# Kernel optimization log

Hardware: AMD Instinct MI355X
Metric: run time of the kernel (lower is better)

Reference implementation:

```python
import jax, jax.numpy as jnp
import numpy as np

N, E, F_IN, H, C, L = 100000, 1600000, 128, 64, 16, 3
NEG_SLOPE_ATT = 0.2   # GATConv attention leaky_relu
NEG_SLOPE_ACT = 0.01  # F.leaky_relu default


def setup_inputs() -> dict:
    key = jax.random.key(0)
    ks = jax.random.split(key, 12)
    x = jax.random.normal(ks[0], (N, F_IN), dtype=jnp.float32)
    edge_index = jax.random.randint(ks[1], (2, E), 0, N, dtype=jnp.int64)
    edge_weight = jax.random.uniform(ks[2], (E,), dtype=jnp.float32)
    s = 0.05
    W_in = jax.random.normal(ks[3], (F_IN, H), dtype=jnp.float32) * s
    b_in = jnp.zeros((H,), dtype=jnp.float32)
    Wc = jax.random.normal(ks[4], (L, H, H), dtype=jnp.float32) * s
    a_src = jax.random.normal(ks[5], (L, H), dtype=jnp.float32) * s
    a_dst = jax.random.normal(ks[6], (L, H), dtype=jnp.float32) * s
    bc = jnp.zeros((L, H), dtype=jnp.float32)
    W_out = jax.random.normal(ks[7], (H, C), dtype=jnp.float32) * s
    b_out = jnp.zeros((C,), dtype=jnp.float32)
    return {"x": x, "edge_index": edge_index, "edge_weight": edge_weight,
            "W_in": W_in, "b_in": b_in, "Wc": Wc, "a_src": a_src,
            "a_dst": a_dst, "bc": bc, "W_out": W_out, "b_out": b_out}


def _gat_layer(h, src, dst, W, asrc, adst, b):
    # linear transform (no bias on lin in PyG GATConv)
    h = h @ W                                   # [N, H]
    # per-node attention contributions
    alpha_s = h @ asrc                          # [N]
    alpha_d = h @ adst                          # [N]
    e = jax.nn.leaky_relu(alpha_s[src] + alpha_d[dst], NEG_SLOPE_ATT)  # [E']
    # segment softmax over destination nodes
    m = jax.ops.segment_max(e, dst, num_segments=N)
    ex = jnp.exp(e - m[dst])
    denom = jax.ops.segment_sum(ex, dst, num_segments=N)
    w = ex / (denom[dst] + 1e-16)
    # weighted scatter-add aggregation
    out = jax.ops.segment_sum(h[src] * w[:, None], dst, num_segments=N)
    return out + b


def reference(x, edge_index, edge_weight, W_in, b_in, Wc, a_src, a_dst, bc, W_out, b_out):
    # add self-loops (PyG GATConv default)
    loops = jnp.arange(N, dtype=edge_index.dtype)
    src = jnp.concatenate([edge_index[0], loops])
    dst = jnp.concatenate([edge_index[1], loops])

    h = jax.nn.leaky_relu(x @ W_in + b_in, NEG_SLOPE_ACT)
    for l in range(L):
        h = jax.nn.leaky_relu(_gat_layer(h, src, dst, Wc[l], a_src[l], a_dst[l], bc[l]), NEG_SLOPE_ACT)
    logits = h @ W_out + b_out
    return jax.nn.log_softmax(logits, axis=-1)
```

## Files before the change

kernel.cpp:

```cpp
#include <hip/hip_runtime.h>

#define N_NODES 100000
#define E_EDGES 1600000
#define F_IN    128
#define H_DIM   64
#define C_OUT   16
#define L_LAYERS 3
#define NTOT    (E_EDGES + N_NODES)
#define MAXD    64

#define BKN2    512
#define NB2     ((N_NODES + BKN2 - 1) / BKN2)
#define BCAP    9216
#define CH      8192
#define PB      ((E_EDGES + CH - 1) / CH)

typedef __attribute__((ext_vector_type(8))) short short8;
typedef __attribute__((ext_vector_type(4))) float f32x4;

__device__ inline unsigned short f2bf(float f) {
    unsigned u = __float_as_uint(f);
    return (unsigned short)((u + 0x7FFFu + ((u >> 16) & 1u)) >> 16);
}
__device__ inline float bf_lo(unsigned p) { return __uint_as_float(p << 16); }
__device__ inline float bf_hi(unsigned p) { return __uint_as_float(p & 0xFFFF0000u); }
__device__ inline unsigned cvt_pk_bf16(float lo, float hi) {
    unsigned r;
    asm("v_cvt_pk_bf16_f32 %0, %1, %2" : "=v"(r) : "v"(lo), "v"(hi));
    return r;
}

__global__ __launch_bounds__(256) void bucket_scatter2(
        const void* __restrict__ eidx,
        int* __restrict__ bcur, unsigned int* __restrict__ packed) {
    __shared__ int cnt[NB2], basel[NB2], curl[NB2], gbase[NB2];
    __shared__ int sd[256];
    __shared__ int sflag;
    __shared__ unsigned int stage[CH];
    __shared__ unsigned char bkt[CH];
    int t = threadIdx.x;
    int b0 = blockIdx.x * CH;
    int ne = min(CH, E_EDGES - b0);
    if (t == 0) sflag = 0;
    for (int i = t; i < NB2; i += 256) cnt[i] = 0;
    __syncthreads();
    {
        int nsamp = min(ne, 1024);
        int any = 0;
        for (int j = t; j < nsamp; j += 256)
            if (((const unsigned*)eidx)[2 * (size_t)(b0 + j) + 1] != 0u) any = 1;
        if (any) atomicOr(&sflag, 1);
    }
    __syncthreads();
    int f64 = sflag ? 0 : 1;

    int es[CH / 256], ed[CH / 256];
    #pragma unroll
    for (int j = 0; j < CH / 256; ++j) {
        int idx = b0 + j * 256 + t;
        if (idx < E_EDGES) {
            if (f64) {
                es[j] = (int)((const long long*)eidx)[idx];
                ed[j] = (int)((const long long*)eidx)[E_EDGES + idx];
            } else {
                es[j] = ((const int*)eidx)[idx];
                ed[j] = ((const int*)eidx)[E_EDGES + idx];
            }
            atomicAdd(&cnt[ed[j] >> 9], 1);
        } else { es[j] = -1; }
    }
    __syncthreads();
    int v = (t < NB2) ? cnt[t] : 0;
    sd[t] = v;
    __syncthreads();
    for (int off = 1; off < 256; off <<= 1) {
        int u = (t >= off) ? sd[t - off] : 0;
        __syncthreads();
        sd[t] += u;
        __syncthreads();
    }
    if (t < NB2) {
        basel[t] = sd[t] - v;
        curl[t] = 0;
        gbase[t] = atomicAdd(&bcur[t], v);
    }
    __syncthreads();
    #pragma unroll
    for (int j = 0; j < CH / 256; ++j) {
        if (es[j] >= 0) {
            int b = ed[j] >> 9;
            int r = atomicAdd(&curl[b], 1);
            int pos = basel[b] + r;
            stage[pos] = ((unsigned)(ed[j] & (BKN2 - 1)) << 17) | (unsigned)es[j];
            bkt[pos] = (unsigned char)b;
        }
    }
    __syncthreads();
    for (int i = t; i < ne; i += 256) {
        int b = bkt[i];
        packed[(size_t)b * BCAP + gbase[b] + (i - basel[b])] = stage[i];
    }
}

__global__ __launch_bounds__(256) void csr_build2(
        const unsigned int* __restrict__ packed, const int* __restrict__ bcur,
        int* __restrict__ row_ptr, int* __restrict__ csr_src) {
    __shared__ int cnt[BKN2], scn[BKN2], cur[BKN2];
    int b = blockIdx.x, t = threadIdx.x;
    scn[t] = (t < b) ? bcur[t] : 0;
    __syncthreads();
    for (int off = 128; off >= 1; off >>= 1) {
        if (t < off) scn[t] += scn[t + off];
        __syncthreads();
    }
    int ebase_b = scn[0];
    __syncthreads();

    int nbase = b * BKN2;
    int nn = min(BKN2, N_NODES - nbase);
    int ec = bcur[b];
    size_t pbase = (size_t)b * BCAP;
    int cbase = ebase_b + nbase;
    cnt[t] = (t < nn) ? 1 : 0;
    cnt[t + 256] = (t + 256 < nn) ? 1 : 0;
    __syncthreads();
    for (int i = t; i < ec; i += 256)
        atomicAdd(&cnt[packed[pbase + i] >> 17], 1);
    __syncthreads();
    scn[t] = cnt[t];
    scn[t + 256] = cnt[t + 256];
    __syncthreads();
    for (int off = 1; off < BKN2; off <<= 1) {
        int u0 = (t >= off) ? scn[t - off] : 0;
        int u1 = (t + 256 >= off) ? scn[t + 256 - off] : 0;
        __syncthreads();
        scn[t] += u0;
        scn[t + 256] += u1;
        __syncthreads();
    }
    #pragma unroll
    for (int q = 0; q < 2; ++q) {
        int idx = t + q * 256;
        if (idx < nn) {
            int offi = scn[idx] - cnt[idx];
            row_ptr[nbase + idx] = cbase + offi;
            csr_src[cbase + offi] = nbase + idx;
            cur[idx] = offi + 1;
        }
    }
    if (b == NB2 - 1 && t == 0) row_ptr[N_NODES] = cbase + ec + nn;
    __syncthreads();
    for (int i = t; i < ec; i += 256) {
        unsigned p = packed[pbase + i];
        int dl = p >> 17, s = (int)(p & 0x1FFFFu);
        int pos = atomicAdd(&cur[dl], 1);
        csr_src[cbase + pos] = s;
    }
}

#define SAW 136

__global__ __launch_bounds__(256) void gemm_in_mfma(
        const float* __restrict__ X, const float* __restrict__ W,
        const float* __restrict__ bias, unsigned* __restrict__ C) {
    __shared__ __align__(16) unsigned short sA[64][SAW];
    __shared__ __align__(16) unsigned short sWT[64][SAW];
    __shared__ float sB[64];
    int t = threadIdx.x;
    int r0 = blockIdx.x * 64;
    #pragma unroll
    for (int it = 0; it < 8; ++it) {
        int idx = it * 256 + t;
        int r = idx >> 5, c4 = (idx & 31) * 4;
        int gr = r0 + r;
        float4 v = make_float4(0.f, 0.f, 0.f, 0.f);
        if (gr < N_NODES) v = *(const float4*)&X[(size_t)gr * F_IN + c4];
        unsigned* dst = (unsigned*)&sA[r][c4];
        dst[0] = cvt_pk_bf16(v.x, v.y);
        dst[1] = cvt_pk_bf16(v.z, v.w);
    }
    #pragma unroll
    for (int it = 0; it < 8; ++it) {
        int idx = it * 256 + t;
        int k = idx >> 4, j4 = (idx & 15) * 4;
        float4 v = *(const float4*)&W[k * 64 + j4];
        sWT[j4 + 0][k] = f2bf(v.x);
        sWT[j4 + 1][k] = f2bf(v.y);
        sWT[j4 + 2][k] = f2bf(v.z);
        sWT[j4 + 3][k] = f2bf(v.w);
    }
    if (t < 64) sB[t] = bias[t];
    __syncthreads();

    int wave = t >> 6, lane = t & 63;
    int cj = lane & 15, kq = lane >> 4;
    int lrow = wave * 16 + cj;
    f32x4 zero = {0.f, 0.f, 0.f, 0.f};
    f32x4 acc[4] = {zero, zero, zero, zero};
    #pragma unroll
    for (int q = 0; q < 4; ++q) {
        short8 a = *(const short8*)&sA[lrow][q * 32 + kq * 8];
        #pragma unroll
        for (int ct = 0; ct < 4; ++ct) {
            short8 bfr = *(const short8*)&sWT[ct * 16 + cj][q * 32 + kq * 8];
            acc[ct] = __builtin_amdgcn_mfma_f32_16x16x32_bf16(a, bfr, acc[ct], 0, 0, 0);
        }
    }
    __syncthreads();
    float* tl = (float*)&sA[0][0] + wave * (16 * 65);
    #pragma unroll
    for (int ct = 0; ct < 4; ++ct) {
        float bsv = sB[ct * 16 + cj];
        #pragma unroll
        for (int r = 0; r < 4; ++r) {
            float v = acc[ct][r] + bsv;
            v = v > 0.f ? v : 0.01f * v;
            tl[(kq * 4 + r) * 65 + ct * 16 + cj] = v;
        }
    }
    unsigned ur[8];
    int trow = lane >> 2, tcb = lane & 3;
    #pragma unroll
    for (int i = 0; i < 8; ++i) {
        float2 fp = *(const float2*)&tl[trow * 65 + tcb * 16 + i * 2];
        ur[i] = cvt_pk_bf16(fp.x, fp.y);
    }
    int grow = r0 + wave * 16 + trow;
    if (grow < N_NODES) {
        uint4* dst = (uint4*)&C[(size_t)grow * 32 + tcb * 8];
        dst[0] = make_uint4(ur[0], ur[1], ur[2], ur[3]);
        dst[1] = make_uint4(ur[4], ur[5], ur[6], ur[7]);
    }
}

__global__ __launch_bounds__(256) void gemm_mfma_kernel(
        const unsigned* __restrict__ A32, const float* __restrict__ W,
        const float* __restrict__ asrc, const float* __restrict__ adst,
        unsigned* __restrict__ C, float* __restrict__ as_, float* __restrict__ ad_) {
    __shared__ __align__(16) unsigned short sWT[64][72];
    __shared__ float sAv[64], sDv[64];
    __shared__ __align__(16) float sTile[4][16 * 65];
    int t = threadIdx.x;
    for (int i = t; i < 64 * 64; i += 256) {
        int k = i >> 6, j = i & 63;
        sWT[j][k] = f2bf(W[i]);
    }
    if (t < 64) { sAv[t] = asrc[t]; sDv[t] = adst[t]; }
    __syncthreads();

    int wave = t >> 6, lane = t & 63;
    int r0 = blockIdx.x * 64 + wave * 16;
    int cj = lane & 15, kq = lane >> 4;

    int ra = r0 + cj;
    if (ra >= N_NODES) ra = N_NODES - 1;
    const short8* arow = (const short8*)&A32[(size_t)ra * 32];
    short8 a0 = arow[kq];
    short8 a1 = arow[4 + kq];

    f32x4 zero = {0.f, 0.f, 0.f, 0.f};
    f32x4 acc[4] = {zero, zero, zero, zero};
    #pragma unroll
    for (int ct = 0; ct < 4; ++ct) {
        short8 b0 = *(const short8*)&sWT[16 * ct + cj][kq * 8];
        short8 b1 = *(const short8*)&sWT[16 * ct + cj][32 + kq * 8];
        acc[ct] = __builtin_amdgcn_mfma_f32_16x16x32_bf16(a0, b0, acc[ct], 0, 0, 0);
        acc[ct] = __builtin_amdgcn_mfma_f32_16x16x32_bf16(a1, b1, acc[ct], 0, 0, 0);
    }

    float av[4], dv[4];
    #pragma unroll
    for (int ct = 0; ct < 4; ++ct) { av[ct] = sAv[ct * 16 + cj]; dv[ct] = sDv[ct * 16 + cj]; }
    #pragma unroll
    for (int r = 0; r < 4; ++r) {
        float ds = acc[0][r] * av[0] + acc[1][r] * av[1] + acc[2][r] * av[2] + acc[3][r] * av[3];
        float dd = acc[0][r] * dv[0] + acc[1][r] * dv[1] + acc[2][r] * dv[2] + acc[3][r] * dv[3];
        #pragma unroll
        for (int off = 1; off < 16; off <<= 1) {
            ds += __shfl_xor(ds, off);
            dd += __shfl_xor(dd, off);
        }
        int grow = r0 + kq * 4 + r;
        if (cj == 0 && grow < N_NODES) { as_[grow] = ds; ad_[grow] = dd; }
    }

    float* tl = sTile[wave];
    #pragma unroll
    for (int ct = 0; ct < 4; ++ct)
        #pragma unroll
        for (int r = 0; r < 4; ++r)
            tl[(kq * 4 + r) * 65 + ct * 16 + cj] = acc[ct][r];
    unsigned ur[8];
    int trow = lane >> 2, tcb = lane & 3;
    #pragma unroll
    for (int i = 0; i < 8; ++i) {
        float2 fp = *(const float2*)&tl[trow * 65 + tcb * 16 + i * 2];
        ur[i] = cvt_pk_bf16(fp.x, fp.y);
    }
    int grow = r0 + trow;
    if (grow < N_NODES) {
        uint4* dst = (uint4*)&C[(size_t)grow * 32 + tcb * 8];
        dst[0] = make_uint4(ur[0], ur[1], ur[2], ur[3]);
        dst[1] = make_uint4(ur[4], ur[5], ur[6], ur[7]);
    }
}

__global__ __launch_bounds__(256) void agg_kernel(
        const int* __restrict__ row_ptr, const int* __restrict__ csr_src,
        const float* __restrict__ as_, const float* __restrict__ ad_,
        const unsigned* __restrict__ hw32, const float* __restrict__ bc,
        unsigned* __restrict__ hout32) {
    __shared__ float exbuf[4][MAXD];
    __shared__ int   sbuf[4][MAXD];
    int wave = threadIdx.x >> 6, lane = threadIdx.x & 63;
    int node = blockIdx.x * 4 + wave;
    if (node >= N_NODES) return;
    int rs = row_ptr[node], re = row_ptr[node + 1];
    int deg = re - rs;
    float aD = ad_[node];
    float psum = 0.f;
    for (int i = lane; i < deg; i += 64) {
        int s = csr_src[rs + i];
        float v = as_[s] + aD;
        v = v > 0.f ? v : 0.2f * v;
        float p = __expf(v);
        if (deg <= MAXD) { exbuf[wave][i] = p; sbuf[wave][i] = s; }
        psum += p;
    }
    #pragma unroll
    for (int off = 32; off >= 1; off >>= 1) psum += __shfl_xor(psum, off);
    float inv = 1.f / (psum + 1e-16f);

    int g = lane >> 4, fl16 = lane & 15;
    float a0 = 0.f, a1 = 0.f, a2 = 0.f, a3 = 0.f;
    if (deg <= MAXD) {
        int i = g;
        for (; i + 4 < deg; i += 8) {
            float w0 = exbuf[wave][i], w1 = exbuf[wave][i + 4];
            int s0 = sbuf[wave][i], s1 = sbuf[wave][i + 4];
            uint2 p0 = *(const uint2*)&hw32[((unsigned)s0 << 5) | (fl16 * 2)];
            uint2 p1 = *(const uint2*)&hw32[((unsigned)s1 << 5) | (fl16 * 2)];
            a0 += w0 * bf_lo(p0.x) + w1 * bf_lo(p1.x);
            a1 += w0 * bf_hi(p0.x) + w1 * bf_hi(p1.x);
            a2 += w0 * bf_lo(p0.y) + w1 * bf_lo(p1.y);
            a3 += w0 * bf_hi(p0.y) + w1 * bf_hi(p1.y);
        }
        for (; i < deg; i += 4) {
            float w = exbuf[wave][i];
            int s = sbuf[wave][i];
            uint2 p = *(const uint2*)&hw32[((unsigned)s << 5) | (fl16 * 2)];
            a0 += w * bf_lo(p.x);
            a1 += w * bf_hi(p.x);
            a2 += w * bf_lo(p.y);
            a3 += w * bf_hi(p.y);
        }
    } else {
        for (int i = g; i < deg; i += 4) {
            int s = csr_src[rs + i];
            float v = as_[s] + aD;
            v = v > 0.f ? v : 0.2f * v;
            float w = __expf(v);
            uint2 p = *(const uint2*)&hw32[((unsigned)s << 5) | (fl16 * 2)];
            a0 += w * bf_lo(p.x);
            a1 += w * bf_hi(p.x);
            a2 += w * bf_lo(p.y);
            a3 += w * bf_hi(p.y);
        }
    }
    a0 += __shfl_xor(a0, 16); a0 += __shfl_xor(a0, 32);
    a1 += __shfl_xor(a1, 16); a1 += __shfl_xor(a1, 32);
    a2 += __shfl_xor(a2, 16); a2 += __shfl_xor(a2, 32);
    a3 += __shfl_xor(a3, 16); a3 += __shfl_xor(a3, 32);
    if (g == 0) {
        float4 bv = *(const float4*)&bc[fl16 * 4];
        float v0 = a0 * inv + bv.x; v0 = v0 > 0.f ? v0 : 0.01f * v0;
        float v1 = a1 * inv + bv.y; v1 = v1 > 0.f ? v1 : 0.01f * v1;
        float v2 = a2 * inv + bv.z; v2 = v2 > 0.f ? v2 : 0.01f * v2;
        float v3 = a3 * inv + bv.w; v3 = v3 > 0.f ? v3 : 0.01f * v3;
        *(uint2*)&hout32[((unsigned)node << 5) | (fl16 * 2)] =
            make_uint2(cvt_pk_bf16(v0, v1), cvt_pk_bf16(v2, v3));
    }
}

__global__ __launch_bounds__(256) void out_logsoftmax_kernel(
        const unsigned* __restrict__ h32, const float* __restrict__ W,
        const float* __restrict__ b, float* __restrict__ out) {
    __shared__ float sW[H_DIM * C_OUT];
    __shared__ float sh[16][H_DIM];
    __shared__ float sb[C_OUT];
    int t = threadIdx.x;
    for (int i = t; i < H_DIM * C_OUT; i += 256) sW[i] = W[i];
    if (t < C_OUT) sb[t] = b[t];
    int row0 = blockIdx.x * 16;
    #pragma unroll
    for (int it = 0; it < 2; ++it) {
        int idx = it * 256 + t;
        int r = idx >> 5, c2 = idx & 31;
        unsigned u = h32[((unsigned)(row0 + r) << 5) | c2];
        sh[r][c2 * 2] = bf_lo(u);
        sh[r][c2 * 2 + 1] = bf_hi(u);
    }
    __syncthreads();
    int r = t >> 4, c = t & 15;
    float acc = sb[c];
    #pragma unroll
    for (int k = 0; k < H_DIM; ++k) acc += sh[r][k] * sW[k * C_OUT + c];
    float m = acc;
    #pragma unroll
    for (int off = 8; off >= 1; off >>= 1) m = fmaxf(m, __shfl_xor(m, off, 16));
    float e = __expf(acc - m);
    float ssum = e;
    #pragma unroll
    for (int off = 8; off >= 1; off >>= 1) ssum += __shfl_xor(ssum, off, 16);
    out[(row0 + r) * C_OUT + c] = acc - m - __logf(ssum);
}

extern "C" void kernel_launch(void* const* d_in, const int* in_sizes, int n_in,
                              void* d_out, int out_size, void* d_ws, size_t ws_size,
                              hipStream_t stream) {
    const float* x     = (const float*)d_in[0];
    const void*  eidx  = d_in[1];
    const float* W_in  = (const float*)d_in[3];
    const float* b_in  = (const float*)d_in[4];
    const float* Wc    = (const float*)d_in[5];
    const float* a_src = (const float*)d_in[6];
    const float* a_dst = (const float*)d_in[7];
    const float* bc    = (const float*)d_in[8];
    const float* W_out = (const float*)d_in[9];
    const float* b_out = (const float*)d_in[10];
    float* out = (float*)d_out;

    unsigned* h     = (unsigned*)d_ws;
    unsigned* hw    = h + (size_t)N_NODES * 32;
    float* as_      = (float*)(hw + (size_t)N_NODES * 32);
    float* ad_      = as_ + N_NODES;
    int*   row_ptr  = (int*)(ad_ + N_NODES);
    int*   csr_src  = row_ptr + N_NODES + 1;
    unsigned int* packed = (unsigned int*)(csr_src + NTOT);
    int*   bcur     = (int*)(packed + (size_t)NB2 * BCAP);

    hipMemsetAsync(bcur, 0, NB2 * sizeof(int), stream);
    bucket_scatter2<<<PB, 256, 0, stream>>>(eidx, bcur, packed);
    csr_build2<<<NB2, 256, 0, stream>>>(packed, bcur, row_ptr, csr_src);

    gemm_in_mfma<<<(N_NODES + 63) / 64, 256, 0, stream>>>(x, W_in, b_in, h);

    unsigned* hin = h;
    unsigned* hx  = hw;
    int mblocks = (N_NODES + 63) / 64;
    for (int l = 0; l < L_LAYERS; ++l) {
        gemm_mfma_kernel<<<mblocks, 256, 0, stream>>>(
            hin, Wc + l * H_DIM * H_DIM,
            a_src + l * H_DIM, a_dst + l * H_DIM, hx, as_, ad_);
        agg_kernel<<<(N_NODES + 3) / 4, 256, 0, stream>>>(
            row_ptr, csr_src, as_, ad_, hx, bc + l * H_DIM, hin);
    }

    out_logsoftmax_kernel<<<N_NODES / 16, 256, 0, stream>>>(hin, W_out, b_out, out);
}
```

Baseline: 297.5 us.

## Fuse input GEMM with first layer GEMM and fold output head into last aggregation

Merges the input projection and the layer-0 linear/attention-score GEMM into one kernel, keeping the intermediate activation tile in shared memory as bf16. It also folds the output linear and log-softmax into the final aggregation kernel through a template flag, and unrolls the aggregation gather loop to four neighbours per iteration. This removes two launches and two round trips of the node feature matrix through global memory. In exchange it uses much more shared memory in the fused GEMM, which may lower occupancy, and the last aggregation kernel must load the output weights in every block.

```diff
diff --git a/kernel.cpp b/kernel.cpp
--- a/kernel.cpp
+++ b/kernel.cpp
@@ -160,12 +160,21 @@
 
 #define SAW 136
 
-__global__ __launch_bounds__(256) void gemm_in_mfma(
-        const float* __restrict__ X, const float* __restrict__ W,
-        const float* __restrict__ bias, unsigned* __restrict__ C) {
-    __shared__ __align__(16) unsigned short sA[64][SAW];
-    __shared__ __align__(16) unsigned short sWT[64][SAW];
-    __shared__ float sB[64];
+__global__ __launch_bounds__(256) void k0_fused(
+        const float* __restrict__ X, const float* __restrict__ Win,
+        const float* __restrict__ bias, const float* __restrict__ Wc0,
+        const float* __restrict__ asrc, const float* __restrict__ adst,
+        unsigned* __restrict__ C, float* __restrict__ as_, float* __restrict__ ad_) {
+    __shared__ __align__(16) unsigned char smem[54208];
+    unsigned short (*sX)[SAW]   = (unsigned short(*)[SAW])smem;
+    unsigned short (*sWTin)[SAW]= (unsigned short(*)[SAW])(smem + 17408);
+    unsigned short (*sWT1)[72]  = (unsigned short(*)[72])(smem + 34816);
+    unsigned short (*sH)[72]    = (unsigned short(*)[72])(smem + 44032);
+    float* sB  = (float*)(smem + 53248);
+    float* sAv = sB + 64;
+    float* sDv = sAv + 64;
+    float* sTile = (float*)smem;
+
     int t = threadIdx.x;
     int r0 = blockIdx.x * 64;
     #pragma unroll
@@ -175,7 +184,7 @@
         int gr = r0 + r;
         float4 v = make_float4(0.f, 0.f, 0.f, 0.f);
         if (gr < N_NODES) v = *(const float4*)&X[(size_t)gr * F_IN + c4];
-        unsigned* dst = (unsigned*)&sA[r][c4];
+        unsigned* dst = (unsigned*)&sX[r][c4];
         dst[0] = cvt_pk_bf16(v.x, v.y);
         dst[1] = cvt_pk_bf16(v.z, v.w);
     }
@@ -183,13 +192,17 @@
     for (int it = 0; it < 8; ++it) {
         int idx = it * 256 + t;
         int k = idx >> 4, j4 = (idx & 15) * 4;
-        float4 v = *(const float4*)&W[k * 64 + j4];
-        sWT[j4 + 0][k] = f2bf(v.x);
-        sWT[j4 + 1][k] = f2bf(v.y);
-        sWT[j4 + 2][k] = f2bf(v.z);
-        sWT[j4 + 3][k] = f2bf(v.w);
-    }
-    if (t < 64) sB[t] = bias[t];
+        float4 v = *(const float4*)&Win[k * 64 + j4];
+        sWTin[j4 + 0][k] = f2bf(v.x);
+        sWTin[j4 + 1][k] = f2bf(v.y);
+        sWTin[j4 + 2][k] = f2bf(v.z);
+        sWTin[j4 + 3][k] = f2bf(v.w);
+    }
+    for (int i = t; i < 64 * 64; i += 256) {
+        int k = i >> 6, j = i & 63;
+        sWT1[j][k] = f2bf(Wc0[i]);
+    }
+    if (t < 64) { sB[t] = bias[t]; sAv[t] = asrc[t]; sDv[t] = adst[t]; }
     __syncthreads();
 
     int wave = t >> 6, lane = t & 63;
@@ -199,15 +212,14 @@
     f32x4 acc[4] = {zero, zero, zero, zero};
     #pragma unroll
     for (int q = 0; q < 4; ++q) {
-        short8 a = *(const short8*)&sA[lrow][q * 32 + kq * 8];
+        short8 a = *(const short8*)&sX[lrow][q * 32 + kq * 8];
         #pragma unroll
         for (int ct = 0; ct < 4; ++ct) {
-            short8 bfr = *(const short8*)&sWT[ct * 16 + cj][q * 32 + kq * 8];
+            short8 bfr = *(const short8*)&sWTin[ct * 16 + cj][q * 32 + kq * 8];
             acc[ct] = __builtin_amdgcn_mfma_f32_16x16x32_bf16(a, bfr, acc[ct], 0, 0, 0);
         }
     }
-    __syncthreads();
-    float* tl = (float*)&sA[0][0] + wave * (16 * 65);
+    unsigned short (*sHw)[72] = &sH[wave * 16];
     #pragma unroll
     for (int ct = 0; ct < 4; ++ct) {
         float bsv = sB[ct * 16 + cj];
@@ -215,9 +227,42 @@
         for (int r = 0; r < 4; ++r) {
             float v = acc[ct][r] + bsv;
             v = v > 0.f ? v : 0.01f * v;
-            tl[(kq * 4 + r) * 65 + ct * 16 + cj] = v;
-        }
-    }
+            sHw[kq * 4 + r][ct * 16 + cj] = f2bf(v);
+        }
+    }
+    short8 a0 = *(const short8*)&sHw[cj][kq * 8];
+    short8 a1 = *(const short8*)&sHw[cj][32 + kq * 8];
+    f32x4 acc2[4] = {zero, zero, zero, zero};
+    #pragma unroll
+    for (int ct = 0; ct < 4; ++ct) {
+        short8 b0 = *(const short8*)&sWT1[16 * ct + cj][kq * 8];
+        short8 b1 = *(const short8*)&sWT1[16 * ct + cj][32 + kq * 8];
+        acc2[ct] = __builtin_amdgcn_mfma_f32_16x16x32_bf16(a0, b0, acc2[ct], 0, 0, 0);
+        acc2[ct] = __builtin_amdgcn_mfma_f32_16x16x32_bf16(a1, b1, acc2[ct], 0, 0, 0);
+    }
+    float av[4], dv[4];
+    #pragma unroll
+    for (int ct = 0; ct < 4; ++ct) { av[ct] = sAv[ct * 16 + cj]; dv[ct] = sDv[ct * 16 + cj]; }
+    int wr0 = r0 + wave * 16;
+    #pragma unroll
+    for (int r = 0; r < 4; ++r) {
+        float ds = acc2[0][r] * av[0] + acc2[1][r] * av[1] + acc2[2][r] * av[2] + acc2[3][r] * av[3];
+        float dd = acc2[0][r] * dv[0] + acc2[1][r] * dv[1] + acc2[2][r] * dv[2] + acc2[3][r] * dv[3];
+        #pragma unroll
+        for (int off = 1; off < 16; off <<= 1) {
+            ds += __shfl_xor(ds, off);
+            dd += __shfl_xor(dd, off);
+        }
+        int grow = wr0 + kq * 4 + r;
+        if (cj == 0 && grow < N_NODES) { as_[grow] = ds; ad_[grow] = dd; }
+    }
+    __syncthreads();
+    float* tl = sTile + wave * (16 * 65);
+    #pragma unroll
+    for (int ct = 0; ct < 4; ++ct)
+        #pragma unroll
+        for (int r = 0; r < 4; ++r)
+            tl[(kq * 4 + r) * 65 + ct * 16 + cj] = acc2[ct][r];
     unsigned ur[8];
     int trow = lane >> 2, tcb = lane & 3;
     #pragma unroll
@@ -225,7 +270,7 @@
         float2 fp = *(const float2*)&tl[trow * 65 + tcb * 16 + i * 2];
         ur[i] = cvt_pk_bf16(fp.x, fp.y);
     }
-    int grow = r0 + wave * 16 + trow;
+    int grow = wr0 + trow;
     if (grow < N_NODES) {
         uint4* dst = (uint4*)&C[(size_t)grow * 32 + tcb * 8];
         dst[0] = make_uint4(ur[0], ur[1], ur[2], ur[3]);
@@ -305,14 +350,26 @@
     }
 }
 
+template<bool FUSE_OUT>
 __global__ __launch_bounds__(256) void agg_kernel(
         const int* __restrict__ row_ptr, const int* __restrict__ csr_src,
         const float* __restrict__ as_, const float* __restrict__ ad_,
         const unsigned* __restrict__ hw32, const float* __restrict__ bc,
-        unsigned* __restrict__ hout32) {
+        unsigned* __restrict__ hout32,
+        const float* __restrict__ Wo, const float* __restrict__ bo,
+        float* __restrict__ out) {
     __shared__ float exbuf[4][MAXD];
     __shared__ int   sbuf[4][MAXD];
+    __shared__ float sh[4][64];
+    __shared__ float sWo[64 * 16];
+    __shared__ float sbo[16];
     int wave = threadIdx.x >> 6, lane = threadIdx.x & 63;
+    int t = threadIdx.x;
+    if (FUSE_OUT) {
+        for (int i = t; i < 64 * 16; i += 256) sWo[i] = Wo[i];
+        if (t < 16) sbo[t] = bo[t];
+        __syncthreads();
+    }
     int node = blockIdx.x * 4 + wave;
     if (node >= N_NODES) return;
     int rs = row_ptr[node], re = row_ptr[node + 1];
@@ -335,15 +392,19 @@
     float a0 = 0.f, a1 = 0.f, a2 = 0.f, a3 = 0.f;
     if (deg <= MAXD) {
         int i = g;
-        for (; i + 4 < deg; i += 8) {
-            float w0 = exbuf[wave][i], w1 = exbuf[wave][i + 4];
-            int s0 = sbuf[wave][i], s1 = sbuf[wave][i + 4];
+        for (; i + 12 < deg; i += 16) {
+            float w0 = exbuf[wave][i],      w1 = exbuf[wave][i + 4];
+            float w2 = exbuf[wave][i + 8],  w3 = exbuf[wave][i + 12];
+            int s0 = sbuf[wave][i],     s1 = sbuf[wave][i + 4];
+            int s2 = sbuf[wave][i + 8], s3 = sbuf[wave][i + 12];
             uint2 p0 = *(const uint2*)&hw32[((unsigned)s0 << 5) | (fl16 * 2)];
             uint2 p1 = *(const uint2*)&hw32[((unsigned)s1 << 5) | (fl16 * 2)];
-            a0 += w0 * bf_lo(p0.x) + w1 * bf_lo(p1.x);
-            a1 += w0 * bf_hi(p0.x) + w1 * bf_hi(p1.x);
-            a2 += w0 * bf_lo(p0.y) + w1 * bf_lo(p1.y);
-            a3 += w0 * bf_hi(p0.y) + w1 * bf_hi(p1.y);
+            uint2 p2 = *(const uint2*)&hw32[((unsigned)s2 << 5) | (fl16 * 2)];
+            uint2 p3 = *(const uint2*)&hw32[((unsigned)s3 << 5) | (fl16 * 2)];
+            a0 += w0 * bf_lo(p0.x) + w1 * bf_lo(p1.x) + w2 * bf_lo(p2.x) + w3 * bf_lo(p3.x);
+            a1 += w0 * bf_hi(p0.x) + w1 * bf_hi(p1.x) + w2 * bf_hi(p2.x) + w3 * bf_hi(p3.x);
+            a2 += w0 * bf_lo(p0.y) + w1 * bf_lo(p1.y) + w2 * bf_lo(p2.y) + w3 * bf_lo(p3.y);
+            a3 += w0 * bf_hi(p0.y) + w1 * bf_hi(p1.y) + w2 * bf_hi(p2.y) + w3 * bf_hi(p3.y);
         }
         for (; i < deg; i += 4) {
             float w = exbuf[wave][i];
@@ -377,42 +438,31 @@
         float v1 = a1 * inv + bv.y; v1 = v1 > 0.f ? v1 : 0.01f * v1;
         float v2 = a2 * inv + bv.z; v2 = v2 > 0.f ? v2 : 0.01f * v2;
         float v3 = a3 * inv + bv.w; v3 = v3 > 0.f ? v3 : 0.01f * v3;
-        *(uint2*)&hout32[((unsigned)node << 5) | (fl16 * 2)] =
-            make_uint2(cvt_pk_bf16(v0, v1), cvt_pk_bf16(v2, v3));
-    }
-}
-
-__global__ __launch_bounds__(256) void out_logsoftmax_kernel(
-        const unsigned* __restrict__ h32, const float* __restrict__ W,
-        const float* __restrict__ b, float* __restrict__ out) {
-    __shared__ float sW[H_DIM * C_OUT];
-    __shared__ float sh[16][H_DIM];
-    __shared__ float sb[C_OUT];
-    int t = threadIdx.x;
-    for (int i = t; i < H_DIM * C_OUT; i += 256) sW[i] = W[i];
-    if (t < C_OUT) sb[t] = b[t];
-    int row0 = blockIdx.x * 16;
-    #pragma unroll
-    for (int it = 0; it < 2; ++it) {
-        int idx = it * 256 + t;
-        int r = idx >> 5, c2 = idx & 31;
-        unsigned u = h32[((unsigned)(row0 + r) << 5) | c2];
-        sh[r][c2 * 2] = bf_lo(u);
-        sh[r][c2 * 2 + 1] = bf_hi(u);
-    }
-    __syncthreads();
-    int r = t >> 4, c = t & 15;
-    float acc = sb[c];
-    #pragma unroll
-    for (int k = 0; k < H_DIM; ++k) acc += sh[r][k] * sW[k * C_OUT + c];
-    float m = acc;
-    #pragma unroll
-    for (int off = 8; off >= 1; off >>= 1) m = fmaxf(m, __shfl_xor(m, off, 16));
-    float e = __expf(acc - m);
-    float ssum = e;
-    #pragma unroll
-    for (int off = 8; off >= 1; off >>= 1) ssum += __shfl_xor(ssum, off, 16);
-    out[(row0 + r) * C_OUT + c] = acc - m - __logf(ssum);
+        if (FUSE_OUT) {
+            sh[wave][fl16 * 4 + 0] = v0;
+            sh[wave][fl16 * 4 + 1] = v1;
+            sh[wave][fl16 * 4 + 2] = v2;
+            sh[wave][fl16 * 4 + 3] = v3;
+        } else {
+            *(uint2*)&hout32[((unsigned)node << 5) | (fl16 * 2)] =
+                make_uint2(cvt_pk_bf16(v0, v1), cvt_pk_bf16(v2, v3));
+        }
+    }
+    if (FUSE_OUT) {
+        if (g == 0) {
+            float acc = sbo[fl16];
+            #pragma unroll 8
+            for (int k = 0; k < 64; ++k) acc += sh[wave][k] * sWo[k * 16 + fl16];
+            float m = acc;
+            #pragma unroll
+            for (int off = 8; off >= 1; off >>= 1) m = fmaxf(m, __shfl_xor(m, off, 16));
+            float e = __expf(acc - m);
+            float ssum = e;
+            #pragma unroll
+            for (int off = 8; off >= 1; off >>= 1) ssum += __shfl_xor(ssum, off, 16);
+            out[(size_t)node * C_OUT + fl16] = acc - m - __logf(ssum);
+        }
+    }
 }
 
 extern "C" void kernel_launch(void* const* d_in, const int* in_sizes, int n_in,
@@ -443,18 +493,22 @@
     bucket_scatter2<<<PB, 256, 0, stream>>>(eidx, bcur, packed);
     csr_build2<<<NB2, 256, 0, stream>>>(packed, bcur, row_ptr, csr_src);
 
-    gemm_in_mfma<<<(N_NODES + 63) / 64, 256, 0, stream>>>(x, W_in, b_in, h);
-
-    unsigned* hin = h;
-    unsigned* hx  = hw;
     int mblocks = (N_NODES + 63) / 64;
-    for (int l = 0; l < L_LAYERS; ++l) {
-        gemm_mfma_kernel<<<mblocks, 256, 0, stream>>>(
-            hin, Wc + l * H_DIM * H_DIM,
-            a_src + l * H_DIM, a_dst + l * H_DIM, hx, as_, ad_);
-        agg_kernel<<<(N_NODES + 3) / 4, 256, 0, stream>>>(
-            row_ptr, csr_src, as_, ad_, hx, bc + l * H_DIM, hin);
-    }
-
-    out_logsoftmax_kernel<<<N_NODES / 16, 256, 0, stream>>>(hin, W_out, b_out, out);
-}
+    k0_fused<<<mblocks, 256, 0, stream>>>(
+        x, W_in, b_in, Wc, a_src, a_dst, hw, as_, ad_);
+
+    int ablocks = (N_NODES + 3) / 4;
+    agg_kernel<false><<<ablocks, 256, 0, stream>>>(
+        row_ptr, csr_src, as_, ad_, hw, bc + 0 * H_DIM, h,
+        nullptr, nullptr, nullptr);
+    gemm_mfma_kernel<<<mblocks, 256, 0, stream>>>(
+        h, Wc + 1 * H_DIM * H_DIM, a_src + 1 * H_DIM, a_dst + 1 * H_DIM, hw, as_, ad_);
+    agg_kernel<false><<<ablocks, 256, 0, stream>>>(
+        row_ptr, csr_src, as_, ad_, hw, bc + 1 * H_DIM, h,
+        nullptr, nullptr, nullptr);
+    gemm_mfma_kernel<<<mblocks, 256, 0, stream>>>(
+        h, Wc + 2 * H_DIM * H_DIM, a_src + 2 * H_DIM, a_dst + 2 * H_DIM, hw, as_, ad_);
+    agg_kernel<true><<<ablocks, 256, 0, stream>>>(
+        row_ptr, csr_src, as_, ad_, hw, bc + 2 * H_DIM, nullptr,
+        W_out, b_out, out);
+}
```

New measurement: 309.2 us. 1.04x slower.
